# Kernel optimization log

Hardware: AMD Instinct MI355X
Metric: run time of the kernel (lower is better)

## Reference

```python
import jax, jax.numpy as jnp
import numpy as np

N, M, D = 16384, 1024, 32


def setup_inputs() -> dict:
    key = jax.random.key(0)
    k1, k2 = jax.random.split(key)
    x = jax.random.normal(k1, (N, D), dtype=jnp.float32)
    centers = jax.random.normal(k2, (M, D), dtype=jnp.float32)
    sigma = jnp.ones((M, D), dtype=jnp.float32)  # get_sigma_ones(s=1.0)
    return {"x": x, "centers": centers, "sigma": sigma}


def reference(x, centers, sigma):
    # Gaussian RBF kernel: exp(-0.5 * delta^T invCov delta) / sqrt((2pi)^D det(S))
    d = x.shape[1]
    s2 = sigma ** 2  # (M, D)
    # invCovMat: inverse of per-center diagonal covariance -> diag(1/s2)
    invCov = jnp.eye(d, dtype=x.dtype) * (1.0 / s2)[:, :, None]  # (M, D, D)
    # denom: sqrt((2pi)^D * prod(s2))
    k = (2.0 * np.pi) ** d  # python float, safe for D=32 in f32
    detS = jnp.sqrt(jnp.asarray(k, x.dtype) * jnp.prod(s2, axis=1))  # (M,)
    delta = x[:, None, :] - centers[None, :, :]  # (N, M, D)
    # batched (1,D) @ (D,D) per (n,m) pair, then elementwise * delta and reduce
    q = jnp.einsum('nmd,mde->nme', delta, invCov)  # (N, M, D)
    X = jnp.sum(q * delta, axis=2)  # (N, M) squared Mahalanobis distance
    return jnp.exp(-0.5 * X) / detS[None, :]  # (N, M)
```

## Files before the change

kernel.cpp:

```cpp
#include <hip/hip_runtime.h>


#define N_  16384
#define M_  1024
#define D_  32
#define NT  64
#define BLK 256

typedef float v2f __attribute__((ext_vector_type(2)));
typedef float v4f __attribute__((ext_vector_type(4)));
#define PIN(v) asm volatile("" : "+v"(v))

__global__ __launch_bounds__(BLK, 4) void rbf_kernel(
    const float* __restrict__ x, const float* __restrict__ centers,
    const float* __restrict__ sigma, float* __restrict__ out)
{
    const int tid = threadIdx.x;
    const int m   = blockIdx.x * BLK + tid;
    const int n0  = blockIdx.y * NT;

    __shared__ __align__(16) float xs[NT * D_];
    __shared__ __align__(16) float r2s[NT];

    {
        const float4* xg  = (const float4*)(x + (size_t)n0 * D_);
        float4*       xsv = (float4*)xs;
        float4 v0 = xg[tid];
        float4 v1 = xg[tid + BLK];
        xsv[tid]       = v0;
        xsv[tid + BLK] = v1;
        float s0 = fmaf(v0.x, v0.x, fmaf(v0.y, v0.y, fmaf(v0.z, v0.z, v0.w * v0.w)));
        float s1 = fmaf(v1.x, v1.x, fmaf(v1.y, v1.y, fmaf(v1.z, v1.z, v1.w * v1.w)));
        #pragma unroll
        for (int off = 1; off < 8; off <<= 1) {
            s0 += __shfl_xor(s0, off);
            s1 += __shfl_xor(s1, off);
        }
        if ((tid & 7) == 0) {
            r2s[tid >> 3]        = s0;
            r2s[(tid >> 3) + 32] = s1;
        }
    }
    __syncthreads();

    const float L2E      = 1.4426950408889634f;
    const float LOG2_2PI = 2.6514961294723187f;

    float s2_0 = 0.f, ld = 0.f;
    bool uf = true;
    {
        const float* sg = sigma + (size_t)m * D_;
        #pragma unroll
        for (int d = 0; d < D_; ++d) {
            float s  = sg[d];
            float s2 = s * s;
            if (d == 0) s2_0 = s2;
            uf = uf && (s2 == s2_0);
            ld += log2f(s2);
        }
    }

    if (__all((int)uf)) {
        const float w0 = 1.0f / s2_0;
        v4f A[D_ / 4];
        float b = 0.f;
        {
            const v4f* cg = (const v4f*)(centers + (size_t)m * D_);
            #pragma unroll
            for (int j = 0; j < D_ / 4; ++j) {
                v4f c = cg[j];
                v4f a = c * w0;
                A[j] = a;
                b = fmaf(c.x, a.x, b);
                b = fmaf(c.y, a.y, b);
                b = fmaf(c.z, a.z, b);
                b = fmaf(c.w, a.w, b);
            }
        }
        #pragma unroll
        for (int j = 0; j < D_ / 4; ++j) PIN(A[j]);

        const float c0 = fmaf(-0.5f * L2E, b, -0.5f * (D_ * LOG2_2PI + ld));
        const float qc = -0.5f * L2E * w0;

        const v4f* r2v = (const v4f*)r2s;
        float* o0 = out + (size_t)n0 * M_ + m;
        #pragma unroll 1
        for (int i = 0; i < NT; i += 4) {
            const v4f* xr = (const v4f*)(xs + (size_t)i * D_);
            v4f acc0 = {0.f,0.f,0.f,0.f}, acc1 = {0.f,0.f,0.f,0.f};
            v4f acc2 = {0.f,0.f,0.f,0.f}, acc3 = {0.f,0.f,0.f,0.f};
            #pragma unroll
            for (int j = 0; j < D_ / 4; ++j) {
                v4f aj = A[j];
                acc0 += xr[j]      * aj;
                acc1 += xr[j + 8]  * aj;
                acc2 += xr[j + 16] * aj;
                acc3 += xr[j + 24] * aj;
            }
            v4f rr = r2v[i >> 2];
            float d0 = (acc0.x + acc0.y) + (acc0.z + acc0.w);
            float d1 = (acc1.x + acc1.y) + (acc1.z + acc1.w);
            float d2 = (acc2.x + acc2.y) + (acc2.z + acc2.w);
            float d3 = (acc3.x + acc3.y) + (acc3.z + acc3.w);
            float f0 = fmaf(L2E, d0, fmaf(qc, rr.x, c0));
            float f1 = fmaf(L2E, d1, fmaf(qc, rr.y, c0));
            float f2 = fmaf(L2E, d2, fmaf(qc, rr.z, c0));
            float f3 = fmaf(L2E, d3, fmaf(qc, rr.w, c0));
            __builtin_nontemporal_store(__builtin_amdgcn_exp2f(f0), o0 + (size_t)(i    ) * M_);
            __builtin_nontemporal_store(__builtin_amdgcn_exp2f(f1), o0 + (size_t)(i + 1) * M_);
            __builtin_nontemporal_store(__builtin_amdgcn_exp2f(f2), o0 + (size_t)(i + 2) * M_);
            __builtin_nontemporal_store(__builtin_amdgcn_exp2f(f3), o0 + (size_t)(i + 3) * M_);
        }
    } else {
        const float c0 = -0.5f * (D_ * LOG2_2PI + ld);
        const float* cg = centers + (size_t)m * D_;
        const float* sg = sigma   + (size_t)m * D_;
        #pragma unroll 1
        for (int i = 0; i < NT; ++i) {
            const float* xr = xs + (size_t)i * D_;
            float a0 = 0.f, a1 = 0.f;
            #pragma unroll
            for (int d = 0; d < D_; d += 2) {
                float s0 = sg[d], s1 = sg[d + 1];
                float t0 = xr[d]     - cg[d];
                float t1 = xr[d + 1] - cg[d + 1];
                a0 = fmaf(t0 * (1.0f / (s0 * s0)), t0, a0);
                a1 = fmaf(t1 * (1.0f / (s1 * s1)), t1, a1);
            }
            float f = fmaf(-0.5f * L2E, a0 + a1, c0);
            out[(size_t)(n0 + i) * M_ + m] = __builtin_amdgcn_exp2f(f);
        }
    }
}

extern "C" void kernel_launch(void* const* d_in, const int* in_sizes, int n_in,
                              void* d_out, int out_size, void* d_ws, size_t ws_size,
                              hipStream_t stream) {
    const float* x = (const float*)d_in[0];
    const float* c = (const float*)d_in[1];
    const float* s = (const float*)d_in[2];
    float* out = (float*)d_out;
    dim3 grid(M_ / BLK, N_ / NT);
    rbf_kernel<<<grid, BLK, 0, stream>>>(x, c, s, out);
}
```

Measured before the change: 96.12 us.

## Read x rows via uniform global loads instead of LDS, halve row tile

Drops the shared-memory staging of the x tile. Each thread now reads x rows straight from global memory at wave-uniform addresses, which the compiler can lower to scalar loads, removing LDS reads from the inner loop. The row tile shrinks from 64 to 32 rows per block, doubling the grid, and the launch-bounds occupancy hint rises from 4 to 6. The risks are scalar-load latency and register pressure in the unrolled 8-row loop, plus more blocks that each recompute the per-center setup.

```diff
diff --git a/kernel.cpp b/kernel.cpp
--- a/kernel.cpp
+++ b/kernel.cpp
@@ -4,14 +4,13 @@
 #define N_  16384
 #define M_  1024
 #define D_  32
-#define NT  64
+#define NT  32
 #define BLK 256
 
-typedef float v2f __attribute__((ext_vector_type(2)));
 typedef float v4f __attribute__((ext_vector_type(4)));
 #define PIN(v) asm volatile("" : "+v"(v))
 
-__global__ __launch_bounds__(BLK, 4) void rbf_kernel(
+__global__ __launch_bounds__(BLK, 6) void rbf_kernel(
     const float* __restrict__ x, const float* __restrict__ centers,
     const float* __restrict__ sigma, float* __restrict__ out)
 {
@@ -19,27 +18,16 @@
     const int m   = blockIdx.x * BLK + tid;
     const int n0  = blockIdx.y * NT;
 
-    __shared__ __align__(16) float xs[NT * D_];
     __shared__ __align__(16) float r2s[NT];
 
     {
-        const float4* xg  = (const float4*)(x + (size_t)n0 * D_);
-        float4*       xsv = (float4*)xs;
-        float4 v0 = xg[tid];
-        float4 v1 = xg[tid + BLK];
-        xsv[tid]       = v0;
-        xsv[tid + BLK] = v1;
-        float s0 = fmaf(v0.x, v0.x, fmaf(v0.y, v0.y, fmaf(v0.z, v0.z, v0.w * v0.w)));
-        float s1 = fmaf(v1.x, v1.x, fmaf(v1.y, v1.y, fmaf(v1.z, v1.z, v1.w * v1.w)));
-        #pragma unroll
-        for (int off = 1; off < 8; off <<= 1) {
-            s0 += __shfl_xor(s0, off);
-            s1 += __shfl_xor(s1, off);
-        }
-        if ((tid & 7) == 0) {
-            r2s[tid >> 3]        = s0;
-            r2s[(tid >> 3) + 32] = s1;
-        }
+        const v4f* xg = (const v4f*)(x + (size_t)n0 * D_);
+        v4f v = xg[tid];
+        float s = fmaf(v.x, v.x, fmaf(v.y, v.y, fmaf(v.z, v.z, v.w * v.w)));
+        s += __shfl_xor(s, 1);
+        s += __shfl_xor(s, 2);
+        s += __shfl_xor(s, 4);
+        if ((tid & 7) == 0) r2s[tid >> 3] = s;
     }
     __syncthreads();
 
@@ -85,32 +73,28 @@
 
         const v4f* r2v = (const v4f*)r2s;
         float* o0 = out + (size_t)n0 * M_ + m;
+
         #pragma unroll 1
-        for (int i = 0; i < NT; i += 4) {
-            const v4f* xr = (const v4f*)(xs + (size_t)i * D_);
-            v4f acc0 = {0.f,0.f,0.f,0.f}, acc1 = {0.f,0.f,0.f,0.f};
-            v4f acc2 = {0.f,0.f,0.f,0.f}, acc3 = {0.f,0.f,0.f,0.f};
+        for (int i = 0; i < NT; i += 8) {
+            v4f ra = r2v[i / 4];
+            v4f rb = r2v[i / 4 + 1];
             #pragma unroll
-            for (int j = 0; j < D_ / 4; ++j) {
-                v4f aj = A[j];
-                acc0 += xr[j]      * aj;
-                acc1 += xr[j + 8]  * aj;
-                acc2 += xr[j + 16] * aj;
-                acc3 += xr[j + 24] * aj;
+            for (int k = 0; k < 8; ++k) {
+                const v4f* row = (const v4f*)(x + (size_t)(n0 + i + k) * D_);
+                v4f x0 = row[0], x1 = row[1], x2 = row[2], x3 = row[3];
+                v4f x4 = row[4], x5 = row[5], x6 = row[6], x7 = row[7];
+                v4f p = x0 * A[0];
+                v4f q = x1 * A[1];
+                p += x2 * A[2];  q += x3 * A[3];
+                p += x4 * A[4];  q += x5 * A[5];
+                p += x6 * A[6];  q += x7 * A[7];
+                v4f t = p + q;
+                float dot = (t.x + t.y) + (t.z + t.w);
+                float rr  = (k < 4) ? ra[k] : rb[k - 4];
+                float f   = fmaf(L2E, dot, fmaf(qc, rr, c0));
+                __builtin_nontemporal_store(__builtin_amdgcn_exp2f(f),
+                                            o0 + (size_t)(i + k) * M_);
             }
-            v4f rr = r2v[i >> 2];
-            float d0 = (acc0.x + acc0.y) + (acc0.z + acc0.w);
-            float d1 = (acc1.x + acc1.y) + (acc1.z + acc1.w);
-            float d2 = (acc2.x + acc2.y) + (acc2.z + acc2.w);
-            float d3 = (acc3.x + acc3.y) + (acc3.z + acc3.w);
-            float f0 = fmaf(L2E, d0, fmaf(qc, rr.x, c0));
-            float f1 = fmaf(L2E, d1, fmaf(qc, rr.y, c0));
-            float f2 = fmaf(L2E, d2, fmaf(qc, rr.z, c0));
-            float f3 = fmaf(L2E, d3, fmaf(qc, rr.w, c0));
-            __builtin_nontemporal_store(__builtin_amdgcn_exp2f(f0), o0 + (size_t)(i    ) * M_);
-            __builtin_nontemporal_store(__builtin_amdgcn_exp2f(f1), o0 + (size_t)(i + 1) * M_);
-            __builtin_nontemporal_store(__builtin_amdgcn_exp2f(f2), o0 + (size_t)(i + 2) * M_);
-            __builtin_nontemporal_store(__builtin_amdgcn_exp2f(f3), o0 + (size_t)(i + 3) * M_);
         }
     } else {
         const float c0 = -0.5f * (D_ * LOG2_2PI + ld);
@@ -118,7 +102,7 @@
         const float* sg = sigma   + (size_t)m * D_;
         #pragma unroll 1
         for (int i = 0; i < NT; ++i) {
-            const float* xr = xs + (size_t)i * D_;
+            const float* xr = x + (size_t)(n0 + i) * D_;
             float a0 = 0.f, a1 = 0.f;
             #pragma unroll
             for (int d = 0; d < D_; d += 2) {
```

New measurement: 96.10 us. Within noise of the previous version (-0.0%).
